# Optimization experiments

Hardware: AMD Instinct MI355X
Metric: run time of the kernel (lower is better)

Reference implementation:

```python
import jax, jax.numpy as jnp
import numpy as np

N, E, B, D, OUT_D = 10000, 160000, 64, 1024, 128

def setup_inputs() -> dict:
    key = jax.random.key(0)
    ks = jax.random.split(key, 18)
    s = 0.02
    return {
        "pro1_x": jax.random.normal(ks[0], (N, D), jnp.float32),
        "pro1_edge_index": jax.random.randint(ks[1], (2, E), 0, N, jnp.int64 if jax.config.jax_enable_x64 else jnp.int32),
        "pro1_batch": jnp.sort(jax.random.randint(ks[2], (N,), 0, B)),
        "pro2_x": jax.random.normal(ks[3], (N, D), jnp.float32),
        "pro2_edge_index": jax.random.randint(ks[4], (2, E), 0, N, jnp.int64 if jax.config.jax_enable_x64 else jnp.int32),
        "pro2_batch": jnp.sort(jax.random.randint(ks[5], (N,), 0, B)),
        "W1": jax.random.normal(ks[6], (D, D), jnp.float32) * s,
        "b1": jnp.zeros((D,), jnp.float32),
        "fc1_W": jax.random.normal(ks[7], (D, OUT_D), jnp.float32) * s,
        "fc1_b": jnp.zeros((OUT_D,), jnp.float32),
        "W2": jax.random.normal(ks[8], (D, D), jnp.float32) * s,
        "b2": jnp.zeros((D,), jnp.float32),
        "fc2_W": jax.random.normal(ks[9], (D, OUT_D), jnp.float32) * s,
        "fc2_b": jnp.zeros((OUT_D,), jnp.float32),
        "final_W": jax.random.normal(ks[10], (2 * OUT_D, 1), jnp.float32) * s,
        "final_b": jnp.zeros((1,), jnp.float32),
    }

def leaky_relu(x):
    return jnp.where(x >= 0, x, 0.01 * x)

def gcn_conv(x, edge_index, W, b):
    # PyG GCNConv with default add_self_loops + symmetric normalization
    src, dst = edge_index[0], edge_index[1]
    h = x @ W  # [N, D]
    deg = jnp.zeros((x.shape[0],), x.dtype).at[dst].add(1.0) + 1.0  # in-degree + self-loop
    dinv = jax.lax.rsqrt(deg)
    norm = dinv[src] * dinv[dst]  # [E]
    agg = jax.ops.segment_sum(h[src] * norm[:, None], dst, num_segments=x.shape[0])
    agg = agg + h * (1.0 / deg)[:, None]  # self-loop contribution: deg^-1/2 * deg^-1/2
    return agg + b

def global_mean_pool(x, batch, num_graphs):
    sums = jax.ops.segment_sum(x, batch, num_segments=num_graphs)
    cnt = jax.ops.segment_sum(jnp.ones((x.shape[0],), x.dtype), batch, num_segments=num_graphs)
    return sums / jnp.maximum(cnt, 1.0)[:, None]

def reference(pro1_x, pro1_edge_index, pro1_batch, pro2_x, pro2_edge_index, pro2_batch,
              W1, b1, fc1_W, fc1_b, W2, b2, fc2_W, fc2_b, final_W, final_b):
    # branch 1
    x = leaky_relu(gcn_conv(pro1_x, pro1_edge_index, W1, b1))
    x = global_mean_pool(x, pro1_batch, B)
    x = leaky_relu(x @ fc1_W + fc1_b)  # dropout is identity in eval
    # branch 2
    xt = leaky_relu(gcn_conv(pro2_x, pro2_edge_index, W2, b2))
    xt = global_mean_pool(xt, pro2_batch, B)
    xt = leaky_relu(xt @ fc2_W + fc2_b)
    combined = jnp.concatenate([x, xt], axis=1)  # [B, 256]
    return combined @ final_W + final_b
```

## Files before the change

### kernel.cpp

```cpp
#include <hip/hip_runtime.h>
#include <stdint.h>

typedef __attribute__((ext_vector_type(8))) short short8;
typedef __attribute__((ext_vector_type(8))) __bf16 bf16x8;
typedef __attribute__((ext_vector_type(4))) float f32x4;

__device__ inline unsigned short f2bf(float f) {
  unsigned u = __float_as_uint(f);
  unsigned r = (u + 0x7FFFu + ((u >> 16) & 1u)) >> 16;
  return (unsigned short)r;
}
__device__ inline float bflo(unsigned v) { return __uint_as_float(v << 16); }
__device__ inline float bfhi(unsigned v) { return __uint_as_float(v & 0xFFFF0000u); }
__device__ inline bf16x8 as_bf(short8 v) { return __builtin_bit_cast(bf16x8, v); }

#define GLOAD_LDS16(gp, lp)                                                   \
  __builtin_amdgcn_global_load_lds(                                           \
      (const __attribute__((address_space(1))) void*)(gp),                    \
      (__attribute__((address_space(3))) void*)(lp), 16, 0, 0)

#define NG 2048
#define NSL 8

__global__ void prep1_kernel(const float* __restrict__ x0, const float* __restrict__ x1,
                             unsigned short* __restrict__ xb0, unsigned short* __restrict__ xb1,
                             const float* __restrict__ W0, const float* __restrict__ W1,
                             unsigned short* __restrict__ Wt0, unsigned short* __restrict__ Wt1,
                             const int* __restrict__ ei0, const int* __restrict__ ei1,
                             int* __restrict__ dg0, int* __restrict__ dg1,
                             int n, int mpad, int E, int CB) {
  __shared__ float tile[32][33];
  int br = blockIdx.y;
  int b = blockIdx.x;
  int t = threadIdx.x;
  if (b < CB) {
    const float* x = br ? x1 : x0;
    unsigned short* xb = br ? xb1 : xb0;
    long i = (long)b * 256 + t;
    long total = (long)mpad * 128;
    if (i >= total) return;
    long e0 = i * 8;
    int row = (int)(e0 >> 10);
    short8 v;
    if (row < n) {
      const float* s = x + e0;
      float4 fa = *(const float4*)(s);
      float4 fb = *(const float4*)(s + 4);
      v[0] = (short)f2bf(fa.x); v[1] = (short)f2bf(fa.y);
      v[2] = (short)f2bf(fa.z); v[3] = (short)f2bf(fa.w);
      v[4] = (short)f2bf(fb.x); v[5] = (short)f2bf(fb.y);
      v[6] = (short)f2bf(fb.z); v[7] = (short)f2bf(fb.w);
    } else {
      v = (short8)0;
    }
    *(short8*)(xb + e0) = v;
  } else if (b < CB + 1024) {
    const float* W = br ? W1 : W0;
    unsigned short* Wt = br ? Wt1 : Wt0;
    int bb = b - CB;
    int bx = bb & 31;
    int by = bb >> 5;
    int tx = t & 31, ty = t >> 5;
#pragma unroll
    for (int r = 0; r < 4; ++r) {
      int k = by * 32 + ty + r * 8;
      tile[ty + r * 8][tx] = W[(long)k * 1024 + bx * 32 + tx];
    }
    __syncthreads();
#pragma unroll
    for (int r = 0; r < 4; ++r) {
      int nrow = bx * 32 + ty + r * 8;
      int kcol = by * 32 + tx;
      Wt[(long)nrow * 1024 + kcol] = f2bf(tile[tx][ty + r * 8]);
    }
  } else {
    const int* ei = br ? ei1 : ei0;
    int* degi = br ? dg1 : dg0;
    int e = (b - CB - 1024) * 256 + t;
    if (e >= E) return;
    atomicAdd(&degi[ei[E + e]], 1);
  }
}

__global__ __launch_bounds__(1024) void scan2_kernel(
    const int* __restrict__ degA, int* __restrict__ offA, int* __restrict__ curA,
    const int* __restrict__ degB, int* __restrict__ offB, int* __restrict__ curB, int n) {
  const int* deg = blockIdx.x ? degB : degA;
  int* off = blockIdx.x ? offB : offA;
  int* cur = blockIdx.x ? curB : curA;
  __shared__ int wsum[17];
  int t = threadIdx.x, lane = t & 63, w = t >> 6;
  int CH = (n + 1023) >> 10;
  int i0 = t * CH;
  int s = 0;
  for (int i = 0; i < CH; ++i) {
    int idx = i0 + i;
    s += (idx < n) ? ((deg[idx] + 4) & ~3) : 0;
  }
  int inc = s;
  for (int d = 1; d < 64; d <<= 1) {
    int x = __shfl_up(inc, d);
    if (lane >= d) inc += x;
  }
  if (lane == 63) wsum[w] = inc;
  __syncthreads();
  if (t == 0) {
    int r = 0;
    for (int k = 0; k < 16; ++k) { int x = wsum[k]; wsum[k] = r; r += x; }
    wsum[16] = r;
  }
  __syncthreads();
  int run = wsum[w] + inc - s;
  for (int i = 0; i < CH; ++i) {
    int idx = i0 + i;
    if (idx < n) {
      off[idx] = run;
      cur[idx] = run;
      run += (deg[idx] + 4) & ~3;
    }
  }
  if (t == 0) off[n] = wsum[16];
}

__global__ void prep2_kernel(const int* __restrict__ ei0, const int* __restrict__ ei1,
                             const int* __restrict__ dg0, const int* __restrict__ dg1,
                             int* __restrict__ cur0, int* __restrict__ cur1,
                             uint2* __restrict__ cw0, uint2* __restrict__ cw1,
                             const int* __restrict__ off0, const int* __restrict__ off1,
                             int* __restrict__ rng0, int* __restrict__ rng1,
                             int E, int N, int FB) {
  int br = blockIdx.y;
  int b = blockIdx.x;
  int t = threadIdx.x;
  if (b < FB) {
    const int* ei = br ? ei1 : ei0;
    const int* dg = br ? dg1 : dg0;
    int* cur = br ? cur1 : cur0;
    uint2* cw = br ? cw1 : cw0;
    int e = b * 256 + t;
    if (e >= E + N) return;
    int s, d; float w;
    if (e < E) {
      s = ei[e]; d = ei[E + e];
      w = rsqrtf((float)(dg[s] + 1)) * rsqrtf((float)(dg[d] + 1));
    } else {
      s = e - E; d = s;
      w = 1.0f / (float)(dg[s] + 1);
    }
    int p = atomicAdd(&cur[d], 1);
    uint2 v; v.x = (unsigned)s * 2048u; v.y = __float_as_uint(w);
    cw[p] = v;
  } else {
    const int* off = br ? off1 : off0;
    int* rng = br ? rng1 : rng0;
    int q = (b - FB) * 256 + t;
    if (q > NG) return;
    if (q == NG) { rng[q] = N; return; }
    long Etot = off[N];
    long target = (long)q * Etot;
    int lo = 0, hi = N;
    while (lo < hi) {
      int mid = (lo + hi) >> 1;
      if ((long)off[mid] * NG >= target) hi = mid; else lo = mid + 1;
    }
    rng[q] = lo;
  }
}

#define BM 128
#define BN 128
#define BK 32

__global__ __launch_bounds__(256) void gemm_bf16_kernel(
    const unsigned short* __restrict__ A0, const unsigned short* __restrict__ A1,
    const unsigned short* __restrict__ B0, const unsigned short* __restrict__ B1,
    unsigned short* __restrict__ C0, unsigned short* __restrict__ C1,
    int M, int Nn, int K) {
  const unsigned short* A = blockIdx.z ? A1 : A0;
  const unsigned short* Bt = blockIdx.z ? B1 : B0;
  unsigned short* C = blockIdx.z ? C1 : C0;
  __shared__ alignas(16) unsigned short As[BM * BK];
  __shared__ alignas(16) unsigned short Bs[BN * BK];
  int t = threadIdx.x;
  int lane = t & 63;
  int w = t >> 6;
  int wm = (w >> 1) * 64, wn = (w & 1) * 64;
  long m0 = (long)blockIdx.x * BM;
  long n0 = (long)blockIdx.y * BN;
  int srow = t >> 2;
  int scol = (t & 3) * 8;
  const unsigned short* Ag = A + (m0 + srow) * K + scol;
  const unsigned short* Bg = Bt + (n0 + srow) * K + scol;
  unsigned short* AsP = As + t * 8;
  unsigned short* BsP = Bs + t * 8;
  int fr = lane & 15;
  int fk = (lane >> 4) * 8;
  const unsigned short* afp = As + (wm + fr) * BK + fk;
  const unsigned short* bfp = Bs + (wn + fr) * BK + fk;
  f32x4 acc[4][4] = {};
  for (int k0 = 0; k0 < K; k0 += BK) {
    __syncthreads();
    GLOAD_LDS16(Ag + k0, AsP);
    GLOAD_LDS16(Ag + (long)64 * K + k0, AsP + 2048);
    GLOAD_LDS16(Bg + k0, BsP);
    GLOAD_LDS16(Bg + (long)64 * K + k0, BsP + 2048);
    __syncthreads();
    short8 af[4], bf[4];
#pragma unroll
    for (int i = 0; i < 4; ++i)
      af[i] = *(const short8*)(afp + i * 16 * BK);
#pragma unroll
    for (int i = 0; i < 4; ++i)
      bf[i] = *(const short8*)(bfp + i * 16 * BK);
#pragma unroll
    for (int i = 0; i < 4; ++i)
#pragma unroll
      for (int j = 0; j < 4; ++j)
        acc[i][j] = __builtin_amdgcn_mfma_f32_16x16x32_bf16(as_bf(af[i]), as_bf(bf[j]),
                                                            acc[i][j], 0, 0, 0);
  }
  int cr = (lane >> 4) * 4;
  int cc = lane & 15;
#pragma unroll
  for (int i = 0; i < 4; ++i)
#pragma unroll
    for (int j = 0; j < 4; ++j) {
      long row = m0 + wm + i * 16 + cr;
      long col = n0 + wn + j * 16 + cc;
      unsigned short* cp = C + row * Nn + col;
#pragma unroll
      for (int r = 0; r < 4; ++r)
        cp[(long)r * Nn] = f2bf(acc[i][j][r]);
    }
}

__global__ __launch_bounds__(256) void agg_pool_kernel(
    const unsigned short* __restrict__ H0, const unsigned short* __restrict__ H1,
    const int* __restrict__ off0, const int* __restrict__ off1,
    const uint2* __restrict__ cw0, const uint2* __restrict__ cw1,
    const int* __restrict__ b0, const int* __restrict__ b1,
    const int* __restrict__ rng0, const int* __restrict__ rng1,
    const float* __restrict__ bias0, const float* __restrict__ bias1,
    float* __restrict__ pool0, float* __restrict__ pool1,
    float* __restrict__ scr0, float* __restrict__ scr1,
    int* __restrict__ gid0, int* __restrict__ gid1) {
  int br = blockIdx.y;
  const uint8_t* Hb = (const uint8_t*)(br ? H1 : H0);
  const int* off = br ? off1 : off0;
  const uint2* cw = br ? cw1 : cw0;
  const int* batch = br ? b1 : b0;
  const int* rng = br ? rng1 : rng0;
  const float* bias = br ? bias1 : bias0;
  float* pool = br ? pool1 : pool0;
  float* scratch = br ? scr1 : scr0;
  int* gid = br ? gid1 : gid0;

  int t = threadIdx.x;
  int wv = t >> 6, lane = t & 63, qw = lane >> 4, l16 = lane & 15;
  int slice = blockIdx.x & 7;
  int part = blockIdx.x >> 3;
  int q = part * 4 + wv;
  int d0 = slice * 128 + l16 * 8;
  unsigned d0b = (unsigned)d0 * 2;
  int na = rng[q], nb = rng[q + 1];
  int g0 = -1, g1 = -1;
  if (na < nb) {
    float4 bv0 = *(const float4*)(bias + d0);
    float4 bv1 = *(const float4*)(bias + d0 + 4);
    float bv[8] = {bv0.x, bv0.y, bv0.z, bv0.w, bv1.x, bv1.y, bv1.z, bv1.w};
    float pacc[8] = {};
    float a[8] = {};
    int curg = batch[na];
    int fi = 0;
    int nd = na;
    int ee = off[na + 1];
    int eend = off[nb];
    int e = off[na];
    uint2 cc = cw[e + qw];
    uint2 cn = cw[e + 4 + qw];
    uint4 hc = *(const uint4*)(Hb + (cc.x + d0b));
#pragma unroll 2
    for (; e < eend; e += 4) {
      uint4 hn = *(const uint4*)(Hb + (cn.x + d0b));
      uint2 c2 = cw[e + 8 + qw];
      float w = __uint_as_float(cc.y);
      a[0] += w * bflo(hc.x); a[1] += w * bfhi(hc.x);
      a[2] += w * bflo(hc.y); a[3] += w * bfhi(hc.y);
      a[4] += w * bflo(hc.z); a[5] += w * bfhi(hc.z);
      a[6] += w * bflo(hc.w); a[7] += w * bfhi(hc.w);
      cc = cn; cn = c2; hc = hn;
      if (e + 4 == ee) {
#pragma unroll
        for (int k = 0; k < 8; ++k) {
          float v = a[k];
          v += __shfl_xor(v, 16);
          v += __shfl_xor(v, 32);
          v += bv[k];
          pacc[k] += (v >= 0.f) ? v : 0.01f * v;
          a[k] = 0.f;
        }
        ++nd;
        if (nd < nb) {
          ee = off[nd + 1];
          int g = batch[nd];
          if (g != curg) {
            if (fi == 0) {
              g0 = curg;
              if (qw == 0) {
                float* sp = scratch + ((long)q * 2 + 0) * 1024 + d0;
                *(float4*)sp = make_float4(pacc[0], pacc[1], pacc[2], pacc[3]);
                *(float4*)(sp + 4) = make_float4(pacc[4], pacc[5], pacc[6], pacc[7]);
              }
            } else {
              if (qw == 0) {
                float* pp = pool + (long)curg * 1024 + d0;
#pragma unroll
                for (int k = 0; k < 8; ++k) atomicAdd(pp + k, pacc[k]);
              }
            }
            ++fi;
#pragma unroll
            for (int k = 0; k < 8; ++k) pacc[k] = 0.f;
            curg = g;
          }
        }
      }
    }
    if (fi == 0) {
      g0 = curg;
      if (qw == 0) {
        float* sp = scratch + ((long)q * 2 + 0) * 1024 + d0;
        *(float4*)sp = make_float4(pacc[0], pacc[1], pacc[2], pacc[3]);
        *(float4*)(sp + 4) = make_float4(pacc[4], pacc[5], pacc[6], pacc[7]);
      }
    } else {
      g1 = curg;
      if (qw == 0) {
        float* sp = scratch + ((long)q * 2 + 1) * 1024 + d0;
        *(float4*)sp = make_float4(pacc[0], pacc[1], pacc[2], pacc[3]);
        *(float4*)(sp + 4) = make_float4(pacc[4], pacc[5], pacc[6], pacc[7]);
      }
    }
  }
  if (slice == 0 && lane == 0) {
    gid[q * 2] = g0;
    gid[q * 2 + 1] = g1;
  }
}

__global__ __launch_bounds__(256) void pool_reduce_kernel(
    const float* __restrict__ scr0, const float* __restrict__ scr1,
    const int* __restrict__ gid0, const int* __restrict__ gid1,
    const int* __restrict__ b0, const int* __restrict__ b1,
    const int* __restrict__ rng0, const int* __restrict__ rng1,
    float* __restrict__ pool0, float* __restrict__ pool1, int N) {
  int br = blockIdx.y;
  const float* scratch = br ? scr1 : scr0;
  const int* gid = br ? gid1 : gid0;
  const int* batch = br ? b1 : b0;
  const int* rng = br ? rng1 : rng0;
  float* pool = br ? pool1 : pool0;
  int g = blockIdx.x >> 2;
  int slice = blockIdx.x & 3;
  int tid = threadIdx.x;
  int lo = 0, hi = N;
  while (lo < hi) { int m = (lo + hi) >> 1; if (batch[m] < g) lo = m + 1; else hi = m; }
  int gs = lo;
  lo = 0; hi = N;
  while (lo < hi) { int m = (lo + hi) >> 1; if (batch[m] <= g) lo = m + 1; else hi = m; }
  int ge = lo;
  if (gs >= ge) return;
  lo = 0; hi = NG - 1;
  while (lo < hi) { int m = (lo + hi) >> 1; if (rng[m + 1] > gs) hi = m; else lo = m + 1; }
  int qlo = lo;
  lo = 0; hi = NG - 1;
  while (lo < hi) { int m = (lo + hi + 1) >> 1; if (rng[m] < ge) lo = m; else hi = m - 1; }
  int qhi = lo;
  float s = 0.f;
  for (int q = qlo; q <= qhi; ++q) {
    int a = gid[q * 2], b = gid[q * 2 + 1];
    if (a == g) s += scratch[((long)q * 2 + 0) * 1024 + slice * 256 + tid];
    if (b == g) s += scratch[((long)q * 2 + 1) * 1024 + slice * 256 + tid];
  }
  long idx = (long)g * 1024 + slice * 256 + tid;
  pool[idx] += s;
}

__global__ __launch_bounds__(256) void fc_final_kernel(
    const float* __restrict__ pool1, const float* __restrict__ pool2,
    const int* __restrict__ b0, const int* __restrict__ b1, int N,
    const float* __restrict__ fc1W, const float* __restrict__ fc1b,
    const float* __restrict__ fc2W, const float* __restrict__ fc2b,
    const float* __restrict__ finW, const float* __restrict__ finb,
    float* __restrict__ out) {
  __shared__ float p1[1024], p2[1024];
  __shared__ float red[256];
  int g = blockIdx.x, t = threadIdx.x;
  int lo = 0, hi = N;
  while (lo < hi) { int m = (lo + hi) >> 1; if (b0[m] < g) lo = m + 1; else hi = m; }
  int gs = lo;
  lo = 0; hi = N;
  while (lo < hi) { int m = (lo + hi) >> 1; if (b0[m] <= g) lo = m + 1; else hi = m; }
  float ic1 = 1.0f / (float)max(lo - gs, 1);
  lo = 0; hi = N;
  while (lo < hi) { int m = (lo + hi) >> 1; if (b1[m] < g) lo = m + 1; else hi = m; }
  gs = lo;
  lo = 0; hi = N;
  while (lo < hi) { int m = (lo + hi) >> 1; if (b1[m] <= g) lo = m + 1; else hi = m; }
  float ic2 = 1.0f / (float)max(lo - gs, 1);
  for (int i = t; i < 1024; i += 256) {
    p1[i] = pool1[(long)g * 1024 + i] * ic1;
    p2[i] = pool2[(long)g * 1024 + i] * ic2;
  }
  __syncthreads();
  float contrib;
  if (t < 128) {
    float a = 0.f;
    for (int k = 0; k < 1024; ++k) a += p1[k] * fc1W[(long)k * 128 + t];
    a += fc1b[t];
    a = a >= 0.f ? a : 0.01f * a;
    contrib = a * finW[t];
  } else {
    int j = t - 128;
    float a = 0.f;
    for (int k = 0; k < 1024; ++k) a += p2[k] * fc2W[(long)k * 128 + j];
    a += fc2b[j];
    a = a >= 0.f ? a : 0.01f * a;
    contrib = a * finW[128 + j];
  }
  red[t] = contrib;
  __syncthreads();
  for (int s = 128; s; s >>= 1) {
    if (t < s) red[t] += red[t + s];
    __syncthreads();
  }
  if (t == 0) out[g] = red[0] + finb[0];
}

extern "C" void kernel_launch(void* const* d_in, const int* in_sizes, int n_in,
                              void* d_out, int out_size, void* d_ws, size_t ws_size,
                              hipStream_t stream) {
  (void)n_in; (void)ws_size;
  const float* xs[2]   = {(const float*)d_in[0], (const float*)d_in[3]};
  const int* eis[2]    = {(const int*)d_in[1], (const int*)d_in[4]};
  const int* bts[2]    = {(const int*)d_in[2], (const int*)d_in[5]};
  const float* Ws[2]   = {(const float*)d_in[6], (const float*)d_in[10]};
  const float* bs[2]   = {(const float*)d_in[7], (const float*)d_in[11]};
  const float* fc1W = (const float*)d_in[8];
  const float* fc1b = (const float*)d_in[9];
  const float* fc2W = (const float*)d_in[12];
  const float* fc2b = (const float*)d_in[13];
  const float* finW = (const float*)d_in[14];
  const float* finb = (const float*)d_in[15];
  float* out = (float*)d_out;

  const int N = in_sizes[2];
  const int E = in_sizes[1] / 2;
  const int Mpad = ((N + 127) / 128) * 128;
  const int CWCAP = E + 4 * N + 64;

  uint8_t* ws = (uint8_t*)d_ws;
  size_t o = 0;
  auto alloc = [&](size_t bytes) { size_t r = o; o += (bytes + 255) & ~(size_t)255; return r; };
  size_t degi_o[2] = {alloc((size_t)N * 4), alloc((size_t)N * 4)};
  size_t pool_o[2] = {alloc((size_t)out_size * 1024 * 4), alloc((size_t)out_size * 1024 * 4)};
  size_t cw_o[2]   = {alloc((size_t)CWCAP * 8), alloc((size_t)CWCAP * 8)};
  size_t zero_end = o;
  size_t cur_o[2]  = {alloc((size_t)N * 4), alloc((size_t)N * 4)};
  size_t off_o[2]  = {alloc((size_t)(N + 1) * 4), alloc((size_t)(N + 1) * 4)};
  size_t rng_o[2]  = {alloc((size_t)(NG + 1) * 4), alloc((size_t)(NG + 1) * 4)};
  size_t gid_o[2]  = {alloc((size_t)NG * 2 * 4), alloc((size_t)NG * 2 * 4)};
  size_t scr_o[2]  = {alloc((size_t)NG * 2 * 1024 * 4), alloc((size_t)NG * 2 * 1024 * 4)};
  size_t xb_o[2]   = {alloc((size_t)Mpad * 1024 * 2), alloc((size_t)Mpad * 1024 * 2)};
  size_t wt_o[2]   = {alloc((size_t)1024 * 1024 * 2), alloc((size_t)1024 * 1024 * 2)};
  size_t h_o[2]    = {alloc((size_t)Mpad * 1024 * 2), alloc((size_t)Mpad * 1024 * 2)};

  (void)hipMemsetAsync(ws, 0, zero_end, stream);

  const int CB = (int)(((long)Mpad * 128 + 255) / 256);
  const int DB = (E + 255) / 256;
  prep1_kernel<<<dim3(CB + 1024 + DB, 2), 256, 0, stream>>>(
      xs[0], xs[1], (unsigned short*)(ws + xb_o[0]), (unsigned short*)(ws + xb_o[1]),
      Ws[0], Ws[1], (unsigned short*)(ws + wt_o[0]), (unsigned short*)(ws + wt_o[1]),
      eis[0], eis[1], (int*)(ws + degi_o[0]), (int*)(ws + degi_o[1]),
      N, Mpad, E, CB);
  scan2_kernel<<<2, 1024, 0, stream>>>(
      (const int*)(ws + degi_o[0]), (int*)(ws + off_o[0]), (int*)(ws + cur_o[0]),
      (const int*)(ws + degi_o[1]), (int*)(ws + off_o[1]), (int*)(ws + cur_o[1]), N);
  const int FB = (E + N + 255) / 256;
  const int RB = (NG + 256) / 256;
  prep2_kernel<<<dim3(FB + RB, 2), 256, 0, stream>>>(
      eis[0], eis[1], (const int*)(ws + degi_o[0]), (const int*)(ws + degi_o[1]),
      (int*)(ws + cur_o[0]), (int*)(ws + cur_o[1]),
      (uint2*)(ws + cw_o[0]), (uint2*)(ws + cw_o[1]),
      (const int*)(ws + off_o[0]), (const int*)(ws + off_o[1]),
      (int*)(ws + rng_o[0]), (int*)(ws + rng_o[1]), E, N, FB);
  gemm_bf16_kernel<<<dim3(Mpad / BM, 1024 / BN, 2), 256, 0, stream>>>(
      (const unsigned short*)(ws + xb_o[0]), (const unsigned short*)(ws + xb_o[1]),
      (const unsigned short*)(ws + wt_o[0]), (const unsigned short*)(ws + wt_o[1]),
      (unsigned short*)(ws + h_o[0]), (unsigned short*)(ws + h_o[1]), Mpad, 1024, 1024);
  agg_pool_kernel<<<dim3((NG / 4) * NSL, 2), 256, 0, stream>>>(
      (const unsigned short*)(ws + h_o[0]), (const unsigned short*)(ws + h_o[1]),
      (const int*)(ws + off_o[0]), (const int*)(ws + off_o[1]),
      (const uint2*)(ws + cw_o[0]), (const uint2*)(ws + cw_o[1]),
      bts[0], bts[1],
      (const int*)(ws + rng_o[0]), (const int*)(ws + rng_o[1]),
      bs[0], bs[1],
      (float*)(ws + pool_o[0]), (float*)(ws + pool_o[1]),
      (float*)(ws + scr_o[0]), (float*)(ws + scr_o[1]),
      (int*)(ws + gid_o[0]), (int*)(ws + gid_o[1]));
  pool_reduce_kernel<<<dim3(out_size * 4, 2), 256, 0, stream>>>(
      (const float*)(ws + scr_o[0]), (const float*)(ws + scr_o[1]),
      (const int*)(ws + gid_o[0]), (const int*)(ws + gid_o[1]),
      bts[0], bts[1],
      (const int*)(ws + rng_o[0]), (const int*)(ws + rng_o[1]),
      (float*)(ws + pool_o[0]), (float*)(ws + pool_o[1]), N);
  fc_final_kernel<<<out_size, 256, 0, stream>>>(
      (const float*)(ws + pool_o[0]), (const float*)(ws + pool_o[1]),
      bts[0], bts[1], N,
      fc1W, fc1b, fc2W, fc2b, finW, finb, out);
}
```

Before: 260.9 us.

## Double GEMM K-tile, swizzle LDS layout, and group block order for L2 reuse

The bf16 MFMA GEMM now stages a 64-wide K slice per iteration instead of 32, which halves the number of barrier pairs per tile. It also adds an XOR swizzle on the LDS column chunks to avoid bank conflicts on fragment reads. Blocks are remapped from a 2D grid to a 1D grid grouped 8 M-tiles by 8 N-tiles for better L2 locality of A and B. In exchange, M padding grows to a multiple of 1024, which adds extra padded rows of GEMM work, and LDS use per block doubles.

```diff
diff --git a/kernel.cpp b/kernel.cpp
--- a/kernel.cpp
+++ b/kernel.cpp
@@ -169,55 +169,67 @@
 
 #define BM 128
 #define BN 128
-#define BK 32
+#define BK 64
 
 __global__ __launch_bounds__(256) void gemm_bf16_kernel(
     const unsigned short* __restrict__ A0, const unsigned short* __restrict__ A1,
     const unsigned short* __restrict__ B0, const unsigned short* __restrict__ B1,
     unsigned short* __restrict__ C0, unsigned short* __restrict__ C1,
-    int M, int Nn, int K) {
+    int Nn, int K) {
   const unsigned short* A = blockIdx.z ? A1 : A0;
   const unsigned short* Bt = blockIdx.z ? B1 : B0;
   unsigned short* C = blockIdx.z ? C1 : C0;
   __shared__ alignas(16) unsigned short As[BM * BK];
   __shared__ alignas(16) unsigned short Bs[BN * BK];
+  int x = blockIdx.x;
+  long m0 = (long)((x >> 6) * 8 + (x & 7)) * BM;
+  long n0 = (long)((x >> 3) & 7) * BN;
   int t = threadIdx.x;
   int lane = t & 63;
   int w = t >> 6;
   int wm = (w >> 1) * 64, wn = (w & 1) * 64;
-  long m0 = (long)blockIdx.x * BM;
-  long n0 = (long)blockIdx.y * BN;
-  int srow = t >> 2;
-  int scol = (t & 3) * 8;
-  const unsigned short* Ag = A + (m0 + srow) * K + scol;
-  const unsigned short* Bg = Bt + (n0 + srow) * K + scol;
+  int l3 = lane >> 3;
+  int gsw = (lane & 7) ^ l3;
+  int srowb = w * 8 + l3;
+  const unsigned short* Ag = A + (m0 + srowb) * K + gsw * 8;
+  const unsigned short* Bg = Bt + (n0 + srowb) * K + gsw * 8;
   unsigned short* AsP = As + t * 8;
   unsigned short* BsP = Bs + t * 8;
   int fr = lane & 15;
-  int fk = (lane >> 4) * 8;
-  const unsigned short* afp = As + (wm + fr) * BK + fk;
-  const unsigned short* bfp = Bs + (wn + fr) * BK + fk;
+  int c0 = (lane >> 4) ^ (lane & 7);
+  const unsigned short* afp0 = As + (wm + fr) * BK + c0 * 8;
+  const unsigned short* afp1 = As + (wm + fr) * BK + (c0 ^ 4) * 8;
+  const unsigned short* bfp0 = Bs + (wn + fr) * BK + c0 * 8;
+  const unsigned short* bfp1 = Bs + (wn + fr) * BK + (c0 ^ 4) * 8;
   f32x4 acc[4][4] = {};
   for (int k0 = 0; k0 < K; k0 += BK) {
     __syncthreads();
-    GLOAD_LDS16(Ag + k0, AsP);
-    GLOAD_LDS16(Ag + (long)64 * K + k0, AsP + 2048);
-    GLOAD_LDS16(Bg + k0, BsP);
-    GLOAD_LDS16(Bg + (long)64 * K + k0, BsP + 2048);
+#pragma unroll
+    for (int j = 0; j < 4; ++j) {
+      GLOAD_LDS16(Ag + (long)(j * 32) * K + k0, AsP + j * 2048);
+      GLOAD_LDS16(Bg + (long)(j * 32) * K + k0, BsP + j * 2048);
+    }
     __syncthreads();
-    short8 af[4], bf[4];
+    short8 af[4][2], bf[4][2];
+#pragma unroll
+    for (int i = 0; i < 4; ++i) {
+      af[i][0] = *(const short8*)(afp0 + i * 16 * BK);
+      af[i][1] = *(const short8*)(afp1 + i * 16 * BK);
+    }
+#pragma unroll
+    for (int i = 0; i < 4; ++i) {
+      bf[i][0] = *(const short8*)(bfp0 + i * 16 * BK);
+      bf[i][1] = *(const short8*)(bfp1 + i * 16 * BK);
+    }
 #pragma unroll
     for (int i = 0; i < 4; ++i)
-      af[i] = *(const short8*)(afp + i * 16 * BK);
-#pragma unroll
-    for (int i = 0; i < 4; ++i)
-      bf[i] = *(const short8*)(bfp + i * 16 * BK);
-#pragma unroll
-    for (int i = 0; i < 4; ++i)
-#pragma unroll
-      for (int j = 0; j < 4; ++j)
-        acc[i][j] = __builtin_amdgcn_mfma_f32_16x16x32_bf16(as_bf(af[i]), as_bf(bf[j]),
+#pragma unroll
+      for (int j = 0; j < 4; ++j) {
+        acc[i][j] = __builtin_amdgcn_mfma_f32_16x16x32_bf16(as_bf(af[i][0]), as_bf(bf[j][0]),
                                                             acc[i][j], 0, 0, 0);
+        acc[i][j] = __builtin_amdgcn_mfma_f32_16x16x32_bf16(as_bf(af[i][1]), as_bf(bf[j][1]),
+                                                            acc[i][j], 0, 0, 0);
+      }
   }
   int cr = (lane >> 4) * 4;
   int cc = lane & 15;
@@ -456,7 +468,8 @@
 
   const int N = in_sizes[2];
   const int E = in_sizes[1] / 2;
-  const int Mpad = ((N + 127) / 128) * 128;
+  const int Mpad = ((N + 1023) / 1024) * 1024;
+  const int MT = Mpad / BM;
   const int CWCAP = E + 4 * N + 64;
 
   uint8_t* ws = (uint8_t*)d_ws;
@@ -495,10 +508,10 @@
       (uint2*)(ws + cw_o[0]), (uint2*)(ws + cw_o[1]),
       (const int*)(ws + off_o[0]), (const int*)(ws + off_o[1]),
       (int*)(ws + rng_o[0]), (int*)(ws + rng_o[1]), E, N, FB);
-  gemm_bf16_kernel<<<dim3(Mpad / BM, 1024 / BN, 2), 256, 0, stream>>>(
+  gemm_bf16_kernel<<<dim3(MT * 8, 1, 2), 256, 0, stream>>>(
       (const unsigned short*)(ws + xb_o[0]), (const unsigned short*)(ws + xb_o[1]),
       (const unsigned short*)(ws + wt_o[0]), (const unsigned short*)(ws + wt_o[1]),
-      (unsigned short*)(ws + h_o[0]), (unsigned short*)(ws + h_o[1]), Mpad, 1024, 1024);
+      (unsigned short*)(ws + h_o[0]), (unsigned short*)(ws + h_o[1]), 1024, 1024);
   agg_pool_kernel<<<dim3((NG / 4) * NSL, 2), 256, 0, stream>>>(
       (const unsigned short*)(ws + h_o[0]), (const unsigned short*)(ws + h_o[1]),
       (const int*)(ws + off_o[0]), (const int*)(ws + off_o[1]),
```

New measurement: 237.3 us. -9.1%, faster.
